# Kernel tuning notes

Measured on AMD Instinct MI355X. Metric: run time of the kernel, lower is better.

Reference implementation:

```python
import jax, jax.numpy as jnp
import numpy as np

N, E, B, IN, DIM, H = 20000, 320000, 128, 25, 64, 8

def _lin(key, fin, fout):
    k1, k2 = jax.random.split(key)
    s = 1.0 / np.sqrt(fin)
    return (jax.random.uniform(k1, (fin, fout), jnp.float32, -s, s),
            jax.random.uniform(k2, (fout,), jnp.float32, -s, s))

def setup_inputs() -> dict:
    key = jax.random.key(0)
    ks = jax.random.split(key, 12)
    x = jax.random.normal(ks[0], (N, IN), jnp.float32)
    edge_index = jax.random.randint(ks[1], (2, E), 0, N, jnp.int64)
    batch = jnp.sort(jax.random.randint(ks[2], (N,), 0, B, jnp.int64))
    W0, b0 = _lin(ks[3], IN, DIM)
    Wg, _ = _lin(ks[4], DIM, H * DIM)            # GATConv lin (no bias)
    att_src = jax.random.normal(ks[5], (H, DIM), jnp.float32) * (1.0 / np.sqrt(DIM))
    att_dst = jax.random.normal(ks[6], (H, DIM), jnp.float32) * (1.0 / np.sqrt(DIM))
    bg = jnp.zeros((H * DIM,), jnp.float32)       # GATConv output bias
    Wh, bh = _lin(ks[7], H * DIM, DIM)            # head_nn
    sl = 1.0 / np.sqrt(DIM)
    W_ih = jax.random.uniform(ks[8], (4 * DIM, 2 * DIM), jnp.float32, -sl, sl)
    W_hh = jax.random.uniform(ks[9], (4 * DIM, DIM), jnp.float32, -sl, sl)
    b_ih = jnp.zeros((4 * DIM,), jnp.float32)
    b_hh = jnp.zeros((4 * DIM,), jnp.float32)
    W1, b1 = _lin(ks[10], 2 * DIM, DIM)
    W2, b2 = _lin(ks[11], DIM, 1)
    return dict(x=x, edge_index=edge_index, batch=batch, W0=W0, b0=b0, Wg=Wg,
                att_src=att_src, att_dst=att_dst, bg=bg, Wh=Wh, bh=bh,
                W_ih=W_ih, W_hh=W_hh, b_ih=b_ih, b_hh=b_hh, W1=W1, b1=b1, W2=W2, b2=b2)

def _forward(x, edge_index, batch, W0, b0, Wg, att_src, att_dst, bg, Wh, bh,
             W_ih, W_hh, b_ih, b_hh, W1, b1, W2, b2):
    n = x.shape[0]
    h0 = jax.nn.relu(x @ W0 + b0)                         # [N, DIM]
    xh = (h0 @ Wg).reshape(n, H, DIM)                     # [N, H, C]
    # add self-loops (PyG GATConv default)
    loop = jnp.arange(n, dtype=edge_index.dtype)
    src = jnp.concatenate([edge_index[0], loop])
    dst = jnp.concatenate([edge_index[1], loop])
    a_s = jnp.einsum('nhc,hc->nh', xh, att_src)           # [N, H]
    a_d = jnp.einsum('nhc,hc->nh', xh, att_dst)
    e = jax.nn.leaky_relu(a_s[src] + a_d[dst], 0.2)       # [Etot, H]
    m = jax.ops.segment_max(e, dst, num_segments=n)
    w = jnp.exp(e - m[dst])
    s = jax.ops.segment_sum(w, dst, num_segments=n)
    alpha = w / s[dst]                                    # segment softmax over dst
    agg = jax.ops.segment_sum(alpha[:, :, None] * xh[src], dst, num_segments=n)
    out = jax.nn.relu(agg.reshape(n, H * DIM) + bg)
    out = jax.nn.relu(out @ Wh + bh)                      # [N, DIM]
    # Set2Set, 3 processing steps
    q_star = jnp.zeros((B, 2 * DIM), out.dtype)
    h = jnp.zeros((B, DIM), out.dtype)
    c = jnp.zeros((B, DIM), out.dtype)
    for _ in range(3):
        g = q_star @ W_ih.T + b_ih + h @ W_hh.T + b_hh
        i_g, f_g, g_g, o_g = jnp.split(g, 4, axis=-1)
        c = jax.nn.sigmoid(f_g) * c + jax.nn.sigmoid(i_g) * jnp.tanh(g_g)
        h = jax.nn.sigmoid(o_g) * jnp.tanh(c)
        q = h                                             # [B, DIM]
        e2 = jnp.sum(out * q[batch], axis=-1)             # [N]
        m2 = jax.ops.segment_max(e2, batch, num_segments=B)
        w2 = jnp.exp(e2 - m2[batch])
        s2 = jax.ops.segment_sum(w2, batch, num_segments=B)
        a2 = w2 / s2[batch]
        r = jax.ops.segment_sum(a2[:, None] * out, batch, num_segments=B)
        q_star = jnp.concatenate([q, r], axis=-1)
    y = jax.nn.relu(q_star @ W1 + b1)
    y = y @ W2 + b2
    return y.reshape(-1)

def reference(x, edge_index, batch, W0, b0, Wg, att_src, att_dst, bg, Wh, bh,
              W_ih, W_hh, b_ih, b_hh, W1, b1, W2, b2):
    return _forward(x, edge_index, batch, W0, b0, Wg, att_src, att_dst, bg, Wh, bh,
                    W_ih, W_hh, b_ih, b_hh, W1, b1, W2, b2)
```

## Files before the change

kernel.cpp:

```cpp
#include <hip/hip_runtime.h>

#define N_NODES 20000
#define N_EDGES 320000
#define NBATCH  128

__device__ __forceinline__ float lrelu(float v) { return v > 0.f ? v : 0.2f * v; }
__device__ __forceinline__ float rdlane(float v, int l) {
    return __int_as_float(__builtin_amdgcn_readlane(__float_as_int(v), l));
}

__global__ void k_h0(const float* __restrict__ x, const float* __restrict__ W0,
                     const float* __restrict__ b0, float* __restrict__ h0,
                     int* __restrict__ deg, int n) {
    __shared__ float ws[25 * 64];
    __shared__ float bs[64];
    __shared__ float xs[100];
    int t = threadIdx.x;
    int gid = blockIdx.x * 256 + t;
    if (gid < n) deg[gid] = 0;
    for (int i = t; i < 25 * 64; i += 256) ws[i] = W0[i];
    if (t < 64) bs[t] = b0[t];
    int nb = blockIdx.x * 4;
    if (t < 100 && nb * 25 + t < n * 25) xs[t] = x[(size_t)nb * 25 + t];
    __syncthreads();
    int node = nb + (t >> 6);
    int c = t & 63;
    if (node >= n) return;
    float s = bs[c];
    const float* xr = xs + (t >> 6) * 25;
    #pragma unroll
    for (int k = 0; k < 25; k++) s += xr[k] * ws[k * 64 + c];
    h0[(size_t)node * 64 + c] = fmaxf(s, 0.f);
}

__global__ void k_small(const float* __restrict__ Wg, const float* __restrict__ att_s,
                        const float* __restrict__ att_d, float* __restrict__ vsd,
                        const int* __restrict__ batch, int* __restrict__ segst, int n, int b) {
    int t = threadIdx.x;
    if (blockIdx.x == 0) {
        int k = t >> 3, h = t & 7;
        const float* wrow = Wg + (size_t)k * 512 + h * 64;
        float s1 = 0.f, s2 = 0.f;
        #pragma unroll 8
        for (int c = 0; c < 64; c++) {
            float w = wrow[c];
            s1 += w * att_s[h * 64 + c];
            s2 += w * att_d[h * 64 + c];
        }
        vsd[k * 16 + h] = s1;
        vsd[k * 16 + 8 + h] = s2;
    } else {
        if (t > b) return;
        int lo = 0, hi = n;
        while (lo < hi) { int mid = (lo + hi) >> 1; if (batch[mid] < t) lo = mid + 1; else hi = mid; }
        segst[t] = lo;
    }
}

__global__ __launch_bounds__(256) void k_asd(const float* __restrict__ h0,
                                             const float* __restrict__ vsd,
                                             float* __restrict__ a_s, float* __restrict__ a_d) {
    __shared__ float hs[16][65];
    __shared__ float vl[64 * 16];
    int tid = threadIdx.x;
    int rbase = blockIdx.x * 16;
    {
        int row = tid / 16, c4 = (tid % 16) * 4;
        float4 hv = *(const float4*)(h0 + (size_t)(rbase + row) * 64 + c4);
        hs[row][c4] = hv.x; hs[row][c4 + 1] = hv.y; hs[row][c4 + 2] = hv.z; hs[row][c4 + 3] = hv.w;
    }
    #pragma unroll
    for (int j = 0; j < 4; j++) vl[tid + j * 256] = vsd[tid + j * 256];
    __syncthreads();
    int nl = tid / 16, o = tid % 16;
    float acc = 0.f;
    #pragma unroll 16
    for (int k = 0; k < 64; k++) acc += hs[nl][k] * vl[k * 16 + o];
    int node = rbase + nl;
    if (o < 8) a_s[node * 8 + o] = acc;
    else       a_d[node * 8 + (o - 8)] = acc;
}

__global__ void k_count(const int* __restrict__ dst, int* __restrict__ deg, int e) {
    int i = blockIdx.x * 256 + threadIdx.x;
    if (i < e) atomicAdd(&deg[dst[i]], 1);
}

__global__ __launch_bounds__(1024) void k_scan1(const int* __restrict__ deg,
                                                int* __restrict__ tmp, int* __restrict__ bsum, int n) {
    __shared__ int wsum[16];
    int tid = threadIdx.x, lane = tid & 63, w = tid >> 6;
    int i = blockIdx.x * 1024 + tid;
    int v = (i < n) ? deg[i] + 1 : 0;
    int x = v;
    #pragma unroll
    for (int off = 1; off < 64; off <<= 1) {
        int t = __shfl_up(x, off);
        if (lane >= off) x += t;
    }
    if (lane == 63) wsum[w] = x;
    __syncthreads();
    int pre = 0;
    #pragma unroll
    for (int j = 0; j < 16; j++) if (j < w) pre += wsum[j];
    if (i < n) tmp[i] = pre + x - v;
    if (tid == 1023) bsum[blockIdx.x] = pre + x;
}

__global__ void k_scan2(const int* __restrict__ tmp, const int* __restrict__ bsum,
                        const float* __restrict__ a_s, const float* __restrict__ a_d,
                        int* __restrict__ offs, int* __restrict__ adj,
                        int* __restrict__ cursor, float* __restrict__ eb, int n, int nblk) {
    int i = blockIdx.x * 256 + threadIdx.x;
    if (i > n) return;
    int b = i >> 10;
    int pre = 0;
    for (int j = 0; j < b; j++) pre += bsum[j];
    if (i == n) {
        int tot = pre;
        for (int j = b; j < nblk; j++) tot += bsum[j];
        offs[n] = tot;
        return;
    }
    int o = pre + tmp[i];
    offs[i] = o;
    adj[o] = i;
    cursor[i] = o + 1;
    float4 s0 = *(const float4*)(a_s + (size_t)i * 8);
    float4 s1 = *(const float4*)(a_s + (size_t)i * 8 + 4);
    float4 d0 = *(const float4*)(a_d + (size_t)i * 8);
    float4 d1 = *(const float4*)(a_d + (size_t)i * 8 + 4);
    float4 e0, e1;
    e0.x = lrelu(s0.x + d0.x); e0.y = lrelu(s0.y + d0.y);
    e0.z = lrelu(s0.z + d0.z); e0.w = lrelu(s0.w + d0.w);
    e1.x = lrelu(s1.x + d1.x); e1.y = lrelu(s1.y + d1.y);
    e1.z = lrelu(s1.z + d1.z); e1.w = lrelu(s1.w + d1.w);
    *(float4*)(eb + (size_t)o * 8) = e0;
    *(float4*)(eb + (size_t)o * 8 + 4) = e1;
}

__global__ void k_fill_edge(const int* __restrict__ src, const int* __restrict__ dst,
                            const float* __restrict__ a_s, const float* __restrict__ a_d,
                            int* __restrict__ cursor, int* __restrict__ adj,
                            float* __restrict__ eb, int e) {
    int i = blockIdx.x * 256 + threadIdx.x;
    if (i >= e) return;
    int s = src[i], d = dst[i];
    int p = atomicAdd(&cursor[d], 1);
    adj[p] = s;
    float4 s0 = *(const float4*)(a_s + (size_t)s * 8);
    float4 s1 = *(const float4*)(a_s + (size_t)s * 8 + 4);
    float4 d0 = *(const float4*)(a_d + (size_t)d * 8);
    float4 d1 = *(const float4*)(a_d + (size_t)d * 8 + 4);
    float4 e0, e1;
    e0.x = lrelu(s0.x + d0.x); e0.y = lrelu(s0.y + d0.y);
    e0.z = lrelu(s0.z + d0.z); e0.w = lrelu(s0.w + d0.w);
    e1.x = lrelu(s1.x + d1.x); e1.y = lrelu(s1.y + d1.y);
    e1.z = lrelu(s1.z + d1.z); e1.w = lrelu(s1.w + d1.w);
    *(float4*)(eb + (size_t)p * 8) = e0;
    *(float4*)(eb + (size_t)p * 8 + 4) = e1;
}

__global__ __launch_bounds__(256) void k_gat4(const int* __restrict__ offs, const int* __restrict__ adj,
                                              const float* __restrict__ eb,
                                              const float* __restrict__ h0,
                                              float* __restrict__ agg_pre, int n) {
    int lane = threadIdx.x & 63;
    int node = blockIdx.x * 4 + (threadIdx.x >> 6);
    if (node >= n) return;
    int beg = offs[node], end = offs[node + 1];
    int g = lane >> 3;

    float m = -1e30f, s = 0.f;
    for (int base = beg; base < end; base += 8) {
        if (base + g < end) {
            float ev = eb[(size_t)base * 8 + lane];
            if (ev > m) { s = s * __expf(m - ev) + 1.f; m = ev; }
            else        { s += __expf(ev - m); }
        }
    }
    #pragma unroll
    for (int off = 8; off < 64; off <<= 1) {
        float mo = __shfl_xor(m, off), so = __shfl_xor(s, off);
        float mn = fmaxf(m, mo);
        s = s * __expf(m - mn) + so * __expf(mo - mn);
        m = mn;
    }
    float rcp = 1.f / s;

    float acc[8] = {0.f, 0.f, 0.f, 0.f, 0.f, 0.f, 0.f, 0.f};
    for (int sbase = beg; sbase < end; sbase += 64) {
        int scnt = end - sbase; if (scnt > 64) scnt = 64;
        int srcv = 0;
        if (lane < scnt) srcv = adj[sbase + lane];
        float al[8];
        #pragma unroll
        for (int j = 0; j < 8; j++) {
            int q = j * 8 + g;
            float ev = -1e30f;
            if (q < scnt) ev = eb[(size_t)sbase * 8 + j * 64 + lane];
            al[j] = __expf(ev - m) * rcp;
        }
        #pragma unroll
        for (int j = 0; j < 8; j++) {
            int qb = j * 8;
            if (qb >= scnt) break;
            int sg[8]; float xv[8];
            #pragma unroll
            for (int g2 = 0; g2 < 8; g2++)
                sg[g2] = __builtin_amdgcn_readlane(srcv, qb + g2);
            #pragma unroll
            for (int g2 = 0; g2 < 8; g2++)
                xv[g2] = h0[(size_t)sg[g2] * 64 + lane];
            #pragma unroll
            for (int g2 = 0; g2 < 8; g2++) {
                #pragma unroll
                for (int h2 = 0; h2 < 8; h2++)
                    acc[h2] += rdlane(al[j], g2 * 8 + h2) * xv[g2];
            }
        }
    }
    #pragma unroll
    for (int h2 = 0; h2 < 8; h2++)
        agg_pre[(size_t)node * 512 + h2 * 64 + lane] = acc[h2];
}

__global__ __launch_bounds__(256) void k_fused4(const float* __restrict__ agg_pre,
                                                const float* __restrict__ Wg,
                                                const float* __restrict__ bg,
                                                const float* __restrict__ Wh,
                                                float* __restrict__ part, int M) {
    __shared__ float AB[64 * 68];
    __shared__ float Bs[64 * 64];
    int tid = threadIdx.x;
    int r0 = blockIdx.x * 64;
    int tx = tid & 7;
    int ty = tid >> 3;
    int rr = tid >> 4, c4 = (tid & 15) * 4;
    float4 accO[2][2] = {};
    #pragma unroll
    for (int hh = 0; hh < 2; hh++) {
        int h = blockIdx.y * 2 + hh;
        #pragma unroll
        for (int pp = 0; pp < 4; pp++) {
            int r = rr + pp * 16;
            float4 av = make_float4(0.f, 0.f, 0.f, 0.f);
            if (r0 + r < M) av = *(const float4*)(agg_pre + (size_t)(r0 + r) * 512 + h * 64 + c4);
            *(float4*)&AB[r * 68 + c4] = av;
            *(float4*)&Bs[r * 64 + c4] = *(const float4*)(Wg + (size_t)r * 512 + h * 64 + c4);
        }
        __syncthreads();
        float4 acc1[2][2] = {};
        #pragma unroll 4
        for (int kc = 0; kc < 16; kc++) {
            float4 a0 = *(const float4*)&AB[(ty * 2 + 0) * 68 + kc * 4];
            float4 a1 = *(const float4*)&AB[(ty * 2 + 1) * 68 + kc * 4];
            #pragma unroll
            for (int kk = 0; kk < 4; kk++) {
                float ak0 = (&a0.x)[kk], ak1 = (&a1.x)[kk];
                float4 bL = *(const float4*)&Bs[(kc * 4 + kk) * 64 + tx * 8];
                float4 bH = *(const float4*)&Bs[(kc * 4 + kk) * 64 + tx * 8 + 4];
                acc1[0][0].x += ak0 * bL.x; acc1[0][0].y += ak0 * bL.y; acc1[0][0].z += ak0 * bL.z; acc1[0][0].w += ak0 * bL.w;
                acc1[0][1].x += ak0 * bH.x; acc1[0][1].y += ak0 * bH.y; acc1[0][1].z += ak0 * bH.z; acc1[0][1].w += ak0 * bH.w;
                acc1[1][0].x += ak1 * bL.x; acc1[1][0].y += ak1 * bL.y; acc1[1][0].z += ak1 * bL.z; acc1[1][0].w += ak1 * bL.w;
                acc1[1][1].x += ak1 * bH.x; acc1[1][1].y += ak1 * bH.y; acc1[1][1].z += ak1 * bH.z; acc1[1][1].w += ak1 * bH.w;
            }
        }
        __syncthreads();
        float4 bgL = *(const float4*)(bg + h * 64 + tx * 8);
        float4 bgH = *(const float4*)(bg + h * 64 + tx * 8 + 4);
        #pragma unroll
        for (int i = 0; i < 2; i++) {
            float4 cL, cH;
            cL.x = fmaxf(acc1[i][0].x + bgL.x, 0.f); cL.y = fmaxf(acc1[i][0].y + bgL.y, 0.f);
            cL.z = fmaxf(acc1[i][0].z + bgL.z, 0.f); cL.w = fmaxf(acc1[i][0].w + bgL.w, 0.f);
            cH.x = fmaxf(acc1[i][1].x + bgH.x, 0.f); cH.y = fmaxf(acc1[i][1].y + bgH.y, 0.f);
            cH.z = fmaxf(acc1[i][1].z + bgH.z, 0.f); cH.w = fmaxf(acc1[i][1].w + bgH.w, 0.f);
            *(float4*)&AB[(ty * 2 + i) * 68 + tx * 8] = cL;
            *(float4*)&AB[(ty * 2 + i) * 68 + tx * 8 + 4] = cH;
        }
        #pragma unroll
        for (int pp = 0; pp < 4; pp++) {
            int k = rr + pp * 16;
            *(float4*)&Bs[k * 64 + c4] = *(const float4*)(Wh + (size_t)(h * 64 + k) * 64 + c4);
        }
        __syncthreads();
        #pragma unroll 4
        for (int kc = 0; kc < 16; kc++) {
            float4 a0 = *(const float4*)&AB[(ty * 2 + 0) * 68 + kc * 4];
            float4 a1 = *(const float4*)&AB[(ty * 2 + 1) * 68 + kc * 4];
            #pragma unroll
            for (int kk = 0; kk < 4; kk++) {
                float ak0 = (&a0.x)[kk], ak1 = (&a1.x)[kk];
                float4 bL = *(const float4*)&Bs[(kc * 4 + kk) * 64 + tx * 8];
                float4 bH = *(const float4*)&Bs[(kc * 4 + kk) * 64 + tx * 8 + 4];
                accO[0][0].x += ak0 * bL.x; accO[0][0].y += ak0 * bL.y; accO[0][0].z += ak0 * bL.z; accO[0][0].w += ak0 * bL.w;
                accO[0][1].x += ak0 * bH.x; accO[0][1].y += ak0 * bH.y; accO[0][1].z += ak0 * bH.z; accO[0][1].w += ak0 * bH.w;
                accO[1][0].x += ak1 * bL.x; accO[1][0].y += ak1 * bL.y; accO[1][0].z += ak1 * bL.z; accO[1][0].w += ak1 * bL.w;
                accO[1][1].x += ak1 * bH.x; accO[1][1].y += ak1 * bH.y; accO[1][1].z += ak1 * bH.z; accO[1][1].w += ak1 * bH.w;
            }
        }
        __syncthreads();
    }
    float* Cb = part + (size_t)blockIdx.y * M * 64;
    #pragma unroll
    for (int i = 0; i < 2; i++) {
        int r = r0 + ty * 2 + i;
        if (r >= M) continue;
        *(float4*)(Cb + (size_t)r * 64 + tx * 8) = accO[i][0];
        *(float4*)(Cb + (size_t)r * 64 + tx * 8 + 4) = accO[i][1];
    }
}

#define SROWS 208
__global__ __launch_bounds__(256) void k_s2s(const float* __restrict__ part,
                                             const float* __restrict__ bh,
                                             const int* __restrict__ segst,
                                             const float* __restrict__ W_ih, const float* __restrict__ W_hh,
                                             const float* __restrict__ b_ih, const float* __restrict__ b_hh,
                                             const float* __restrict__ W1, const float* __restrict__ b1,
                                             const float* __restrict__ W2, const float* __restrict__ b2,
                                             float* __restrict__ out, int M) {
    int b = blockIdx.x, tid = threadIdx.x, lane = tid & 63, w = tid >> 6;
    __shared__ float sc[SROWS * 65];
    __shared__ float wlds[1024];
    __shared__ float hl[64], cl[64], rl_[64];
    __shared__ float red[4];
    __shared__ float gsh[256];
    int beg = segst[b], end = segst[b + 1];
    int nrows = end - beg;
    int ncache = nrows < SROWS ? nrows : SROWS;
    const size_t PS = (size_t)M * 64;
    for (int idx = tid; idx < ncache * 16; idx += 256) {
        int r = idx >> 4, q = idx & 15;
        const float* pb = part + (size_t)(beg + r) * 64 + q * 4;
        float4 v0 = *(const float4*)pb;
        float4 v1 = *(const float4*)(pb + PS);
        float4 v2 = *(const float4*)(pb + 2 * PS);
        float4 v3 = *(const float4*)(pb + 3 * PS);
        float4 bv = *(const float4*)(bh + q * 4);
        float* p = &sc[r * 65 + q * 4];
        p[0] = fmaxf(v0.x + v1.x + v2.x + v3.x + bv.x, 0.f);
        p[1] = fmaxf(v0.y + v1.y + v2.y + v3.y + bv.y, 0.f);
        p[2] = fmaxf(v0.z + v1.z + v2.z + v3.z + bv.z, 0.f);
        p[3] = fmaxf(v0.w + v1.w + v2.w + v3.w + bv.w, 0.f);
    }
    if (tid < 64) { hl[tid] = 0.f; cl[tid] = 0.f; rl_[tid] = 0.f; }
    __syncthreads();

    for (int it = 0; it < 3; it++) {
        {
            float acc = b_ih[tid] + b_hh[tid];
            const float* wi = W_ih + (size_t)tid * 128;
            const float* wh = W_hh + (size_t)tid * 64;
            #pragma unroll 8
            for (int k = 0; k < 64; k++) acc += hl[k] * (wi[k] + wh[k]) + rl_[k] * wi[64 + k];
            gsh[tid] = acc;
        }
        __syncthreads();
        if (tid < 64) {
            float ig = gsh[tid], fg = gsh[64 + tid], gg = gsh[128 + tid], og = gsh[192 + tid];
            float cc = cl[tid];
            float si = 1.f / (1.f + __expf(-ig));
            float sf = 1.f / (1.f + __expf(-fg));
            float so = 1.f / (1.f + __expf(-og));
            float cn = sf * cc + si * tanhf(gg);
            cl[tid] = cn;
            hl[tid] = so * tanhf(cn);
        }
        __syncthreads();
        float ev[4];
        int nr = 0;
        float mloc = -1e30f;
        for (int i = tid; i < nrows; i += 256) {
            float d = 0.f;
            if (i < SROWS) {
                const float* rp = &sc[i * 65];
                #pragma unroll 16
                for (int j = 0; j < 64; j++) d += rp[j] * hl[j];
            } else {
                const float* pb = part + (size_t)(beg + i) * 64;
                for (int j = 0; j < 64; j++) {
                    float v = pb[j] + pb[PS + j] + pb[2 * PS + j] + pb[3 * PS + j] + bh[j];
                    d += fmaxf(v, 0.f) * hl[j];
                }
            }
            ev[nr++] = d;
            mloc = fmaxf(mloc, d);
        }
        #pragma unroll
        for (int off = 1; off < 64; off <<= 1) mloc = fmaxf(mloc, __shfl_xor(mloc, off));
        if (lane == 0) red[w] = mloc;
        __syncthreads();
        float m = fmaxf(fmaxf(red[0], red[1]), fmaxf(red[2], red[3]));
        __syncthreads();
        float sloc = 0.f;
        nr = 0;
        for (int i = tid; i < nrows; i += 256) {
            float wv = __expf(ev[nr++] - m);
            if (i < 1024) wlds[i] = wv;
            sloc += wv;
        }
        #pragma unroll
        for (int off = 1; off < 64; off <<= 1) sloc += __shfl_xor(sloc, off);
        if (lane == 0) red[w] = sloc;
        __syncthreads();
        float sv = red[0] + red[1] + red[2] + red[3];
        float inv = sv > 0.f ? 1.f / sv : 0.f;
        float acc = 0.f;
        for (int i = w; i < nrows; i += 4) {
            float v;
            if (i < SROWS) v = sc[i * 65 + lane];
            else {
                const float* pb = part + (size_t)(beg + i) * 64 + lane;
                v = fmaxf(pb[0] + pb[PS] + pb[2 * PS] + pb[3 * PS] + bh[lane], 0.f);
            }
            acc += wlds[i] * v;
        }
        gsh[w * 64 + lane] = acc;
        __syncthreads();
        if (tid < 64)
            rl_[tid] = (gsh[tid] + gsh[64 + tid] + gsh[128 + tid] + gsh[192 + tid]) * inv;
        __syncthreads();
    }
    if (tid < 64) {
        float t = b1[tid];
        #pragma unroll 8
        for (int k = 0; k < 64; k++)
            t += hl[k] * W1[(size_t)k * 64 + tid] + rl_[k] * W1[(size_t)(64 + k) * 64 + tid];
        t = fmaxf(t, 0.f) * W2[tid];
        #pragma unroll
        for (int off = 32; off > 0; off >>= 1) t += __shfl_xor(t, off);
        if (tid == 0) out[b] = t + b2[0];
    }
}

extern "C" void kernel_launch(void* const* d_in, const int* in_sizes, int n_in,
                              void* d_out, int out_size, void* d_ws, size_t ws_size,
                              hipStream_t stream) {
    const float* x     = (const float*)d_in[0];
    const int*   ei    = (const int*)d_in[1];
    const int*   batch = (const int*)d_in[2];
    const float* W0    = (const float*)d_in[3];
    const float* b0    = (const float*)d_in[4];
    const float* Wg    = (const float*)d_in[5];
    const float* att_s = (const float*)d_in[6];
    const float* att_d = (const float*)d_in[7];
    const float* bg    = (const float*)d_in[8];
    const float* Wh    = (const float*)d_in[9];
    const float* bh    = (const float*)d_in[10];
    const float* W_ih  = (const float*)d_in[11];
    const float* W_hh  = (const float*)d_in[12];
    const float* b_ih  = (const float*)d_in[13];
    const float* b_hh  = (const float*)d_in[14];
    const float* W1    = (const float*)d_in[15];
    const float* b1    = (const float*)d_in[16];
    const float* W2    = (const float*)d_in[17];
    const float* b2    = (const float*)d_in[18];
    float* out = (float*)d_out;

    const int* esrc = ei;
    const int* edst = ei + N_EDGES;

    char* wsb = (char*)d_ws;
    size_t off = 0;
    auto alloc = [&](size_t bytes) {
        void* p = wsb + off;
        off = (off + bytes + 255) & ~(size_t)255;
        return p;
    };
    float* h0      = (float*)alloc((size_t)N_NODES * 64 * 4);
    float* agg_pre = (float*)alloc((size_t)N_NODES * 512 * 4);
    float* part    = (float*)alloc((size_t)4 * N_NODES * 64 * 4);
    float* a_s     = (float*)alloc((size_t)N_NODES * 8 * 4);
    float* a_d     = (float*)alloc((size_t)N_NODES * 8 * 4);
    float* vsd     = (float*)alloc(64 * 16 * 4);
    float* eb      = (float*)alloc((size_t)(N_EDGES + N_NODES) * 8 * 4);
    int*   deg     = (int*)alloc((size_t)N_NODES * 4);
    int*   tmp     = (int*)alloc((size_t)N_NODES * 4);
    int*   bsum    = (int*)alloc(32 * 4);
    int*   offs    = (int*)alloc((size_t)(N_NODES + 1) * 4);
    int*   cursor  = (int*)alloc((size_t)N_NODES * 4);
    int*   adj     = (int*)alloc((size_t)(N_EDGES + N_NODES) * 4);
    int*   segst   = (int*)alloc((size_t)(NBATCH + 1) * 4);

    k_h0<<<(N_NODES + 3) / 4, 256, 0, stream>>>(x, W0, b0, h0, deg, N_NODES);
    k_small<<<2, 512, 0, stream>>>(Wg, att_s, att_d, vsd, batch, segst, N_NODES, NBATCH);
    k_asd<<<N_NODES / 16, 256, 0, stream>>>(h0, vsd, a_s, a_d);

    k_count<<<(N_EDGES + 255) / 256, 256, 0, stream>>>(edst, deg, N_EDGES);
    const int nblk = (N_NODES + 1023) / 1024;
    k_scan1<<<nblk, 1024, 0, stream>>>(deg, tmp, bsum, N_NODES);
    k_scan2<<<(N_NODES + 256) / 256, 256, 0, stream>>>(tmp, bsum, a_s, a_d, offs, adj, cursor, eb, N_NODES, nblk);
    k_fill_edge<<<(N_EDGES + 255) / 256, 256, 0, stream>>>(esrc, edst, a_s, a_d, cursor, adj, eb, N_EDGES);

    k_gat4<<<(N_NODES + 3) / 4, 256, 0, stream>>>(offs, adj, eb, h0, agg_pre, N_NODES);
    k_fused4<<<dim3((N_NODES + 63) / 64, 4), 256, 0, stream>>>(agg_pre, Wg, bg, Wh, part, N_NODES);

    k_s2s<<<NBATCH, 256, 0, stream>>>(part, bh, segst, W_ih, W_hh, b_ih, b_hh, W1, b1, W2, b2, out, N_NODES);
}
```

Before: 269.2 us.

## Fuse degree counting, scan and preprocessing kernels; double-batch gathers in GAT

Moves the degree zeroing into the small setup kernel and folds the edge-count atomics into the h0 kernel, with 5000 blocks of 64 atomics covering all 320000 edges. The first scan pass now runs as extra 256-thread blocks inside the a_s/a_d kernel, which removes the standalone count and scan1 launches. The block-sum array grows, and scan2 now loops over up to 79 partial sums per thread. The GAT aggregation loop now issues two groups of 8 neighbour row gathers before accumulating, so more loads are in flight at the cost of extra registers.

```diff
diff --git a/kernel.cpp b/kernel.cpp
--- a/kernel.cpp
+++ b/kernel.cpp
@@ -9,15 +9,45 @@
     return __int_as_float(__builtin_amdgcn_readlane(__float_as_int(v), l));
 }
 
-__global__ void k_h0(const float* __restrict__ x, const float* __restrict__ W0,
-                     const float* __restrict__ b0, float* __restrict__ h0,
-                     int* __restrict__ deg, int n) {
+__global__ void k_small(const float* __restrict__ Wg, const float* __restrict__ att_s,
+                        const float* __restrict__ att_d, float* __restrict__ vsd,
+                        const int* __restrict__ batch, int* __restrict__ segst,
+                        int* __restrict__ deg, int n, int b) {
+    int tid = threadIdx.x;
+    int gid = blockIdx.x * 256 + tid;
+    if (gid < n) deg[gid] = 0;
+    if (blockIdx.x < 2) {
+        int t = blockIdx.x * 256 + tid;
+        int k = t >> 3, h = t & 7;
+        const float* wrow = Wg + (size_t)k * 512 + h * 64;
+        float s1 = 0.f, s2 = 0.f;
+        #pragma unroll 8
+        for (int c = 0; c < 64; c++) {
+            float w = wrow[c];
+            s1 += w * att_s[h * 64 + c];
+            s2 += w * att_d[h * 64 + c];
+        }
+        vsd[k * 16 + h] = s1;
+        vsd[k * 16 + 8 + h] = s2;
+    } else if (blockIdx.x == 2) {
+        if (tid > b) return;
+        int lo = 0, hi = n;
+        while (lo < hi) { int mid = (lo + hi) >> 1; if (batch[mid] < tid) lo = mid + 1; else hi = mid; }
+        segst[tid] = lo;
+    }
+}
+
+__global__ void k_h0c(const float* __restrict__ x, const float* __restrict__ W0,
+                      const float* __restrict__ b0, float* __restrict__ h0,
+                      const int* __restrict__ edst, int* __restrict__ deg, int n) {
     __shared__ float ws[25 * 64];
     __shared__ float bs[64];
     __shared__ float xs[100];
     int t = threadIdx.x;
-    int gid = blockIdx.x * 256 + t;
-    if (gid < n) deg[gid] = 0;
+    if (t < 64) {
+        int e = blockIdx.x * 64 + t;
+        atomicAdd(&deg[edst[e]], 1);
+    }
     for (int i = t; i < 25 * 64; i += 256) ws[i] = W0[i];
     if (t < 64) bs[t] = b0[t];
     int nb = blockIdx.x * 4;
@@ -33,36 +63,36 @@
     h0[(size_t)node * 64 + c] = fmaxf(s, 0.f);
 }
 
-__global__ void k_small(const float* __restrict__ Wg, const float* __restrict__ att_s,
-                        const float* __restrict__ att_d, float* __restrict__ vsd,
-                        const int* __restrict__ batch, int* __restrict__ segst, int n, int b) {
-    int t = threadIdx.x;
-    if (blockIdx.x == 0) {
-        int k = t >> 3, h = t & 7;
-        const float* wrow = Wg + (size_t)k * 512 + h * 64;
-        float s1 = 0.f, s2 = 0.f;
-        #pragma unroll 8
-        for (int c = 0; c < 64; c++) {
-            float w = wrow[c];
-            s1 += w * att_s[h * 64 + c];
-            s2 += w * att_d[h * 64 + c];
-        }
-        vsd[k * 16 + h] = s1;
-        vsd[k * 16 + 8 + h] = s2;
-    } else {
-        if (t > b) return;
-        int lo = 0, hi = n;
-        while (lo < hi) { int mid = (lo + hi) >> 1; if (batch[mid] < t) lo = mid + 1; else hi = mid; }
-        segst[t] = lo;
-    }
-}
-
-__global__ __launch_bounds__(256) void k_asd(const float* __restrict__ h0,
-                                             const float* __restrict__ vsd,
-                                             float* __restrict__ a_s, float* __restrict__ a_d) {
+__global__ __launch_bounds__(256) void k_asd_scan(const float* __restrict__ h0,
+                                                  const float* __restrict__ vsd,
+                                                  float* __restrict__ a_s, float* __restrict__ a_d,
+                                                  const int* __restrict__ deg,
+                                                  int* __restrict__ tmp, int* __restrict__ bsum,
+                                                  int nasd, int n) {
     __shared__ float hs[16][65];
     __shared__ float vl[64 * 16];
+    __shared__ int wsum[4];
     int tid = threadIdx.x;
+    if (blockIdx.x >= nasd) {
+        int s = blockIdx.x - nasd;
+        int i = s * 256 + tid;
+        int lane = tid & 63, w = tid >> 6;
+        int v = (i < n) ? deg[i] + 1 : 0;
+        int x = v;
+        #pragma unroll
+        for (int off = 1; off < 64; off <<= 1) {
+            int t2 = __shfl_up(x, off);
+            if (lane >= off) x += t2;
+        }
+        if (lane == 63) wsum[w] = x;
+        __syncthreads();
+        int pre = 0;
+        #pragma unroll
+        for (int j = 0; j < 4; j++) if (j < w) pre += wsum[j];
+        if (i < n) tmp[i] = pre + x - v;
+        if (tid == 255) bsum[s] = pre + x;
+        return;
+    }
     int rbase = blockIdx.x * 16;
     {
         int row = tid / 16, c4 = (tid % 16) * 4;
@@ -81,39 +111,13 @@
     else       a_d[node * 8 + (o - 8)] = acc;
 }
 
-__global__ void k_count(const int* __restrict__ dst, int* __restrict__ deg, int e) {
-    int i = blockIdx.x * 256 + threadIdx.x;
-    if (i < e) atomicAdd(&deg[dst[i]], 1);
-}
-
-__global__ __launch_bounds__(1024) void k_scan1(const int* __restrict__ deg,
-                                                int* __restrict__ tmp, int* __restrict__ bsum, int n) {
-    __shared__ int wsum[16];
-    int tid = threadIdx.x, lane = tid & 63, w = tid >> 6;
-    int i = blockIdx.x * 1024 + tid;
-    int v = (i < n) ? deg[i] + 1 : 0;
-    int x = v;
-    #pragma unroll
-    for (int off = 1; off < 64; off <<= 1) {
-        int t = __shfl_up(x, off);
-        if (lane >= off) x += t;
-    }
-    if (lane == 63) wsum[w] = x;
-    __syncthreads();
-    int pre = 0;
-    #pragma unroll
-    for (int j = 0; j < 16; j++) if (j < w) pre += wsum[j];
-    if (i < n) tmp[i] = pre + x - v;
-    if (tid == 1023) bsum[blockIdx.x] = pre + x;
-}
-
 __global__ void k_scan2(const int* __restrict__ tmp, const int* __restrict__ bsum,
                         const float* __restrict__ a_s, const float* __restrict__ a_d,
                         int* __restrict__ offs, int* __restrict__ adj,
                         int* __restrict__ cursor, float* __restrict__ eb, int n, int nblk) {
     int i = blockIdx.x * 256 + threadIdx.x;
     if (i > n) return;
-    int b = i >> 10;
+    int b = i >> 8;
     int pre = 0;
     for (int j = 0; j < b; j++) pre += bsum[j];
     if (i == n) {
@@ -161,7 +165,7 @@
     *(float4*)(eb + (size_t)p * 8 + 4) = e1;
 }
 
-__global__ __launch_bounds__(256) void k_gat4(const int* __restrict__ offs, const int* __restrict__ adj,
+__global__ __launch_bounds__(256) void k_gat5(const int* __restrict__ offs, const int* __restrict__ adj,
                                               const float* __restrict__ eb,
                                               const float* __restrict__ h0,
                                               float* __restrict__ agg_pre, int n) {
@@ -202,21 +206,35 @@
             al[j] = __expf(ev - m) * rcp;
         }
         #pragma unroll
-        for (int j = 0; j < 8; j++) {
-            int qb = j * 8;
-            if (qb >= scnt) break;
-            int sg[8]; float xv[8];
+        for (int j = 0; j < 8; j += 2) {
+            int qb0 = j * 8, qb1 = (j + 1) * 8;
+            if (qb0 >= scnt) break;
+            bool has1 = qb1 < scnt;
+            int sg0[8], sg1[8];
+            float xv0[8], xv1[8];
             #pragma unroll
-            for (int g2 = 0; g2 < 8; g2++)
-                sg[g2] = __builtin_amdgcn_readlane(srcv, qb + g2);
+            for (int g2 = 0; g2 < 8; g2++) sg0[g2] = __builtin_amdgcn_readlane(srcv, qb0 + g2);
             #pragma unroll
-            for (int g2 = 0; g2 < 8; g2++)
-                xv[g2] = h0[(size_t)sg[g2] * 64 + lane];
+            for (int g2 = 0; g2 < 8; g2++) sg1[g2] = __builtin_amdgcn_readlane(srcv, qb1 + g2);
+            #pragma unroll
+            for (int g2 = 0; g2 < 8; g2++) xv0[g2] = h0[(size_t)sg0[g2] * 64 + lane];
+            if (has1) {
+                #pragma unroll
+                for (int g2 = 0; g2 < 8; g2++) xv1[g2] = h0[(size_t)sg1[g2] * 64 + lane];
+            }
             #pragma unroll
             for (int g2 = 0; g2 < 8; g2++) {
                 #pragma unroll
                 for (int h2 = 0; h2 < 8; h2++)
-                    acc[h2] += rdlane(al[j], g2 * 8 + h2) * xv[g2];
+                    acc[h2] += rdlane(al[j], g2 * 8 + h2) * xv0[g2];
+            }
+            if (has1) {
+                #pragma unroll
+                for (int g2 = 0; g2 < 8; g2++) {
+                    #pragma unroll
+                    for (int h2 = 0; h2 < 8; h2++)
+                        acc[h2] += rdlane(al[j + 1], g2 * 8 + h2) * xv1[g2];
+                }
             }
         }
     }
@@ -478,23 +496,23 @@
     float* eb      = (float*)alloc((size_t)(N_EDGES + N_NODES) * 8 * 4);
     int*   deg     = (int*)alloc((size_t)N_NODES * 4);
     int*   tmp     = (int*)alloc((size_t)N_NODES * 4);
-    int*   bsum    = (int*)alloc(32 * 4);
+    int*   bsum    = (int*)alloc(128 * 4);
     int*   offs    = (int*)alloc((size_t)(N_NODES + 1) * 4);
     int*   cursor  = (int*)alloc((size_t)N_NODES * 4);
     int*   adj     = (int*)alloc((size_t)(N_EDGES + N_NODES) * 4);
     int*   segst   = (int*)alloc((size_t)(NBATCH + 1) * 4);
 
-    k_h0<<<(N_NODES + 3) / 4, 256, 0, stream>>>(x, W0, b0, h0, deg, N_NODES);
-    k_small<<<2, 512, 0, stream>>>(Wg, att_s, att_d, vsd, batch, segst, N_NODES, NBATCH);
-    k_asd<<<N_NODES / 16, 256, 0, stream>>>(h0, vsd, a_s, a_d);
-
-    k_count<<<(N_EDGES + 255) / 256, 256, 0, stream>>>(edst, deg, N_EDGES);
-    const int nblk = (N_NODES + 1023) / 1024;
-    k_scan1<<<nblk, 1024, 0, stream>>>(deg, tmp, bsum, N_NODES);
-    k_scan2<<<(N_NODES + 256) / 256, 256, 0, stream>>>(tmp, bsum, a_s, a_d, offs, adj, cursor, eb, N_NODES, nblk);
+    const int nscan = (N_NODES + 255) / 256;
+    const int nasd  = N_NODES / 16;
+
+    k_small<<<82, 256, 0, stream>>>(Wg, att_s, att_d, vsd, batch, segst, deg, N_NODES, NBATCH);
+    k_h0c<<<N_NODES / 4, 256, 0, stream>>>(x, W0, b0, h0, edst, deg, N_NODES);
+    k_asd_scan<<<nasd + nscan, 256, 0, stream>>>(h0, vsd, a_s, a_d, deg, tmp, bsum, nasd, N_NODES);
+
+    k_scan2<<<(N_NODES + 256) / 256, 256, 0, stream>>>(tmp, bsum, a_s, a_d, offs, adj, cursor, eb, N_NODES, nscan);
     k_fill_edge<<<(N_EDGES + 255) / 256, 256, 0, stream>>>(esrc, edst, a_s, a_d, cursor, adj, eb, N_EDGES);
 
-    k_gat4<<<(N_NODES + 3) / 4, 256, 0, stream>>>(offs, adj, eb, h0, agg_pre, N_NODES);
+    k_gat5<<<(N_NODES + 3) / 4, 256, 0, stream>>>(offs, adj, eb, h0, agg_pre, N_NODES);
     k_fused4<<<dim3((N_NODES + 63) / 64, 4), 256, 0, stream>>>(agg_pre, Wg, bg, Wh, part, N_NODES);
 
     k_s2s<<<NBATCH, 256, 0, stream>>>(part, bh, segst, W_ih, W_hh, b_ih, b_hh, W1, b1, W2, b2, out, N_NODES);
```

Result: faster. 256.6 us (-4.7%).
